# Optimization experiments

Measured on AMD Instinct MI355X. Metric: run time of the kernel, lower is better.

Reference implementation:

```python
import jax, jax.numpy as jnp
import numpy as np

WIDTH = 384  # reconstruction grid is WIDTH x WIDTH


def _conv2d(x, w, b, pad):
    y = jax.lax.conv_general_dilated(
        x, w, window_strides=(1, 1), padding=[(pad, pad), (pad, pad)],
        dimension_numbers=('NCHW', 'OIHW', 'NCHW'))
    return y + b[None, :, None, None]


def _backproject(sino, angles, width):
    """Pixel-driven flat-detector fan-beam backprojection with linear interp.
    torch-radon FanBeam defaults: src_dist = det_dist = det_count,
    det_spacing = (src_dist + det_dist) / src_dist.
    sino: [B, C, A, D] -> image [B, C, width, width]."""
    B, C, A, D = sino.shape
    dsrc = float(D)
    ddet = float(D)
    spacing = (dsrc + ddet) / dsrc  # = 2.0
    c = jnp.arange(width, dtype=sino.dtype) - (width - 1) / 2.0
    X = c[None, None, :]   # [1,1,W] image x
    Y = c[None, :, None]   # [1,W,1] image y
    cb = jnp.cos(angles)[:, None, None]  # [A,1,1]
    sb = jnp.sin(angles)[:, None, None]
    px = cb * X + sb * Y    # pixel coords in rotated (source) frame, [A,W,W]
    py = -sb * X + cb * Y
    # fractional detector coordinate of the ray source->pixel
    s = px * ((dsrc + ddet) / spacing) / (dsrc + py) + (D - 1) / 2.0
    i0 = jnp.floor(s)
    frac = s - i0
    i0 = i0.astype(jnp.int32)
    i1 = i0 + 1
    WW = width * width
    w0 = jnp.where((i0 >= 0) & (i0 < D), 1.0 - frac, 0.0).reshape(A, WW)
    w1 = jnp.where((i1 >= 0) & (i1 < D), frac, 0.0).reshape(A, WW)
    i0c = jnp.clip(i0, 0, D - 1).reshape(A, WW)
    i1c = jnp.clip(i1, 0, D - 1).reshape(A, WW)

    def gather(idx):
        return jnp.take_along_axis(
            sino, jnp.broadcast_to(idx[None, None], (B, C, A, WW)), axis=3)

    out = (gather(i0c) * w0 + gather(i1c) * w1).sum(axis=2)  # sum over angles
    return out.reshape(B, C, width, width)


def setup_inputs() -> dict:
    key = jax.random.key(0)
    ks = jax.random.split(key, 5)
    A, D = 192, 576
    sino = jax.random.normal(ks[0], (1, 1, A, D), dtype=jnp.float32)
    angles = (jnp.arange(A, dtype=jnp.float32) * (2.0 * np.pi / A))
    w1 = jax.random.normal(ks[1], (16, 1, 5, 5), dtype=jnp.float32) * 0.05
    b1 = jnp.zeros((16,), dtype=jnp.float32)
    w2 = jax.random.normal(ks[2], (1, 16, 5, 5), dtype=jnp.float32) * 0.05
    b2 = jnp.zeros((1,), dtype=jnp.float32)
    w3 = jax.random.normal(ks[3], (1, 2, 3, 3), dtype=jnp.float32) * 0.05
    b3 = jnp.zeros((1,), dtype=jnp.float32)
    return {"sino": sino, "angles": angles, "w1": w1, "b1": b1,
            "w2": w2, "b2": b2, "w3": w3, "b3": b3}


def reference(sino, angles, w1, b1, w2, b2, w3, b3):
    img = _backproject(sino, angles, WIDTH)
    h = _conv2d(sino, w1, b1, pad=2)
    sino_pred = _conv2d(h, w2, b2, pad=2)
    img_sino = _backproject(sino_pred, angles, WIDTH)
    img_pred = _conv2d(jnp.concatenate([img, img_sino], axis=1), w3, b3, pad=1)
    return (sino_pred, img_sino, img_pred)
```

## Files before the change

kernel.cpp:

```cpp
#include <hip/hip_runtime.h>

#define A_N 192
#define D_N 576
#define W_N 384
#define NPIX (W_N * W_N)
#define NSIN (A_N * D_N)
#define RSTR 580

__global__ __launch_bounds__(256) void conv9_kernel(
    const float* __restrict__ sino, const float* __restrict__ angles,
    const float* __restrict__ w1, const float* __restrict__ b1,
    const float* __restrict__ w2, const float* __restrict__ b2,
    float* __restrict__ sino_pred, float2* __restrict__ inter,
    float4* __restrict__ tab)
{
    __shared__ float t[16][40];
    __shared__ float sw1[400], sw2[400], sb1[16];
    __shared__ float K[625], wsb1[25];
    __shared__ float Wcs[9][81];
    __shared__ float biasc[9];

    int tid = threadIdx.x;
    int byi = blockIdx.x / 18;
    int bxi = blockIdx.x % 18;
    int y0 = byi * 8, x0 = bxi * 32;

    if (blockIdx.x == 0) {
        if (tid < A_N) {
            float s, c;
            sincosf(angles[tid], &s, &c);
            tab[tid] = make_float4(c, s, fmaf(576.f, c, -287.5f * s),
                                         fmaf(576.f, s,  287.5f * c));
        }
        for (int i = tid; i < A_N * 4; i += 256) {
            int a = i >> 2, j = i & 3;
            inter[a * RSTR + (j < 2 ? j : 576 + j)] = make_float2(0.f, 0.f);
        }
    }

    for (int i = tid; i < 640; i += 256) {
        int r = i / 40, c = i - r * 40;
        int gy = y0 - 4 + r, gx = x0 - 4 + c;
        t[r][c] = (gy >= 0 && gy < A_N && gx >= 0 && gx < D_N)
                ? sino[gy * D_N + gx] : 0.f;
    }
    for (int i = tid; i < 400; i += 256) { sw1[i] = w1[i]; sw2[i] = w2[i]; }
    if (tid < 16) sb1[tid] = b1[tid];
    __syncthreads();

    for (int i = tid; i < 625; i += 256) {
        int q = i / 25, r = i - q * 25;
        float acc = 0.f;
        #pragma unroll
        for (int c = 0; c < 16; ++c)
            acc = fmaf(sw2[c * 25 + q], sw1[c * 25 + r], acc);
        K[i] = acc;
    }
    if (tid < 25) {
        float acc = 0.f;
        #pragma unroll
        for (int c = 0; c < 16; ++c) acc = fmaf(sw2[c * 25 + tid], sb1[c], acc);
        wsb1[tid] = acc;
    }
    __syncthreads();

    int ylo = (y0 == 0) ? 0 : 2, yhi = (y0 == A_N - 8) ? 4 : 2;
    int xlo = (x0 == 0) ? 0 : 2, xhi = (x0 == D_N - 32) ? 4 : 2;
    int nx = xhi - xlo + 1;
    int nc = (yhi - ylo + 1) * nx;

    for (int e = tid; e < nc * 81; e += 256) {
        int ci = e / 81, s = e - ci * 81;
        int yc = ylo + ci / nx, xc = xlo + ci % nx;
        int sy = s / 9 - 4, sx = s % 9 - 4;
        float acc = 0.f;
        for (int qy = -2; qy <= 2; ++qy) {
            if ((yc == 0 && qy < 0) || (yc == 1 && qy < -1) ||
                (yc == 3 && qy > 1) || (yc == 4 && qy > 0)) continue;
            int vy = sy - qy; if (vy < -2 || vy > 2) continue;
            for (int qx = -2; qx <= 2; ++qx) {
                if ((xc == 0 && qx < 0) || (xc == 1 && qx < -1) ||
                    (xc == 3 && qx > 1) || (xc == 4 && qx > 0)) continue;
                int vx = sx - qx; if (vx < -2 || vx > 2) continue;
                acc += K[((qy + 2) * 5 + qx + 2) * 25 + (vy + 2) * 5 + (vx + 2)];
            }
        }
        Wcs[ci][s] = acc;
    }
    if (tid < nc) {
        int yc = ylo + tid / nx, xc = xlo + tid % nx;
        float acc = b2[0];
        for (int qy = -2; qy <= 2; ++qy) {
            if ((yc == 0 && qy < 0) || (yc == 1 && qy < -1) ||
                (yc == 3 && qy > 1) || (yc == 4 && qy > 0)) continue;
            for (int qx = -2; qx <= 2; ++qx) {
                if ((xc == 0 && qx < 0) || (xc == 1 && qx < -1) ||
                    (xc == 3 && qx > 1) || (xc == 4 && qx > 0)) continue;
                acc += wsb1[(qy + 2) * 5 + qx + 2];
            }
        }
        biasc[tid] = acc;
    }
    __syncthreads();

    int lr = tid >> 5, lc = tid & 31;
    int gy = y0 + lr, gx = x0 + lc;
    int yc = (gy <= 1) ? gy : ((gy >= A_N - 2) ? (gy - (A_N - 5)) : 2);
    int xc = (gx <= 1) ? gx : ((gx >= D_N - 2) ? (gx - (D_N - 5)) : 2);
    int ci = (yc - ylo) * nx + (xc - xlo);
    float acc = biasc[ci];
    const float* Wp = Wcs[ci];
    #pragma unroll
    for (int sy = 0; sy < 9; ++sy)
        #pragma unroll
        for (int sx = 0; sx < 9; ++sx)
            acc = fmaf(t[lr + sy][lc + sx], Wp[sy * 9 + sx], acc);
    sino_pred[gy * D_N + gx] = acc;
    inter[gy * RSTR + 2 + gx] = make_float2(t[lr + 4][lc + 4], acc);
}

__global__ __launch_bounds__(256) void backproject2_kernel(
    const float2* __restrict__ inter, const float4* __restrict__ tab,
    float* __restrict__ part)
{
    int tid = threadIdx.x;
    int seg = blockIdx.z;
    int a0 = seg * 48;
    int tx = tid & 15, ty = tid >> 4;
    int gx = blockIdx.x * 16 + tx;
    int gy = blockIdx.y * 16 + ty;
    int idx = gy * W_N + gx;
    float X = (float)gx - 191.5f;
    float Y = (float)gy - 191.5f;
    float acc0 = 0.f, acc1 = 0.f;
    const float2* base = inter + (size_t)a0 * RSTR + 2;
    #pragma unroll 4
    for (int i = 0; i < 48; ++i) {
        float4 tb = tab[a0 + i];
        float den = fmaf(tb.x, Y, fmaf(-tb.y, X, 576.f));
        float num = fmaf(tb.z, X, fmaf(tb.w, Y, 165600.f));
        float s   = num * __builtin_amdgcn_rcpf(den);
        float fl  = floorf(s);
        float fr  = s - fl;
        int   i0  = (int)fl;
        bool valid = (unsigned)(i0 + 1) <= 577u;
        float w0 = valid ? (1.f - fr) : 0.f;
        float w1 = valid ? fr : 0.f;
        int ic = min(max(i0, -1), 576);
        float4 v = *reinterpret_cast<const float4*>(base + (size_t)i * RSTR + ic);
        acc0 = fmaf(v.x, w0, fmaf(v.z, w1, acc0));
        acc1 = fmaf(v.y, w0, fmaf(v.w, w1, acc1));
    }
    part[seg * NPIX + idx]       = acc0;
    part[(4 + seg) * NPIX + idx] = acc1;
}

__global__ __launch_bounds__(256) void conv3_kernel(
    const float* __restrict__ part,
    const float* __restrict__ w3, const float* __restrict__ b3,
    float* __restrict__ img_sino, float* __restrict__ img_pred)
{
    __shared__ float t0[10][34], t1[10][34];
    __shared__ float sw[18];
    int tid = threadIdx.x;
    int byi = blockIdx.x / 12, bxi = blockIdx.x % 12;
    int y0 = byi * 8, x0 = bxi * 32;
    for (int i = tid; i < 340; i += 256) {
        int r = i / 34, c = i - r * 34;
        int gy = y0 - 1 + r, gx = x0 - 1 + c;
        float s0 = 0.f, s1 = 0.f;
        if (gy >= 0 && gy < W_N && gx >= 0 && gx < W_N) {
            int g = gy * W_N + gx;
            #pragma unroll
            for (int p = 0; p < 4; ++p) s0 += part[p * NPIX + g];
            #pragma unroll
            for (int p = 4; p < 8; ++p) s1 += part[p * NPIX + g];
        }
        t0[r][c] = s0; t1[r][c] = s1;
    }
    if (tid < 18) sw[tid] = w3[tid];
    __syncthreads();
    int lr = tid >> 5, lc = tid & 31;
    int gy = y0 + lr, gx = x0 + lc;
    int g = gy * W_N + gx;
    img_sino[g] = t1[lr + 1][lc + 1];
    float acc = b3[0];
    #pragma unroll
    for (int dy = 0; dy < 3; ++dy)
        #pragma unroll
        for (int dx = 0; dx < 3; ++dx) {
            acc = fmaf(t0[lr + dy][lc + dx], sw[dy * 3 + dx], acc);
            acc = fmaf(t1[lr + dy][lc + dx], sw[9 + dy * 3 + dx], acc);
        }
    img_pred[g] = acc;
}

extern "C" void kernel_launch(void* const* d_in, const int* in_sizes, int n_in,
                              void* d_out, int out_size, void* d_ws, size_t ws_size,
                              hipStream_t stream) {
    const float* sino   = (const float*)d_in[0];
    const float* angles = (const float*)d_in[1];
    const float* w1     = (const float*)d_in[2];
    const float* b1     = (const float*)d_in[3];
    const float* w2     = (const float*)d_in[4];
    const float* b2     = (const float*)d_in[5];
    const float* w3     = (const float*)d_in[6];
    const float* b3     = (const float*)d_in[7];

    float* out       = (float*)d_out;
    float* sino_pred = out;
    float* img_sino  = out + NSIN;
    float* img_pred  = img_sino + NPIX;

    float2* inter = (float2*)d_ws;
    float4* tab   = (float4*)((char*)d_ws + (size_t)A_N * RSTR * sizeof(float2));
    float*  part  = (float*)((char*)tab + A_N * sizeof(float4));

    conv9_kernel<<<dim3(432), dim3(256), 0, stream>>>(
        sino, angles, w1, b1, w2, b2, sino_pred, inter, tab);
    backproject2_kernel<<<dim3(24, 24, 4), dim3(256), 0, stream>>>(
        inter, tab, part);
    conv3_kernel<<<dim3(576), dim3(256), 0, stream>>>(
        part, w3, b3, img_sino, img_pred);
}
```

Before: 38.49 us.

## Split weight-folding into prep kernel and retile backprojection into 8x8 blocks

Moves the per-block 9x9 composite-kernel folding out of conv9 into a single-block prep kernel that writes all 25 boundary-class kernels to global memory; conv9 blocks now just copy the classes they need. Backprojection switches to 64-thread 8x8 pixel tiles with 2 angle segments of 96, which halves the partial buffers that conv3 must sum. The validity branch is dropped by clamping the index to -2 and relying on zero padding columns. This adds a kernel launch and a serialized single-block prep stage, and the clamp assumes out-of-range taps always land on zeroed padding.

Result: slower. 44.47 us (+15.5%).

```diff
diff --git a/kernel.cpp b/kernel.cpp
--- a/kernel.cpp
+++ b/kernel.cpp
@@ -7,47 +7,19 @@
 #define NSIN (A_N * D_N)
 #define RSTR 580
 
-__global__ __launch_bounds__(256) void conv9_kernel(
-    const float* __restrict__ sino, const float* __restrict__ angles,
+__global__ __launch_bounds__(256) void prep_kernel(
+    const float* __restrict__ angles,
     const float* __restrict__ w1, const float* __restrict__ b1,
     const float* __restrict__ w2, const float* __restrict__ b2,
-    float* __restrict__ sino_pred, float2* __restrict__ inter,
-    float4* __restrict__ tab)
-{
-    __shared__ float t[16][40];
+    float4* __restrict__ tab, float2* __restrict__ inter,
+    float* __restrict__ Wc_g, float* __restrict__ biasc_g)
+{
     __shared__ float sw1[400], sw2[400], sb1[16];
     __shared__ float K[625], wsb1[25];
-    __shared__ float Wcs[9][81];
-    __shared__ float biasc[9];
-
-    int tid = threadIdx.x;
-    int byi = blockIdx.x / 18;
-    int bxi = blockIdx.x % 18;
-    int y0 = byi * 8, x0 = bxi * 32;
-
-    if (blockIdx.x == 0) {
-        if (tid < A_N) {
-            float s, c;
-            sincosf(angles[tid], &s, &c);
-            tab[tid] = make_float4(c, s, fmaf(576.f, c, -287.5f * s),
-                                         fmaf(576.f, s,  287.5f * c));
-        }
-        for (int i = tid; i < A_N * 4; i += 256) {
-            int a = i >> 2, j = i & 3;
-            inter[a * RSTR + (j < 2 ? j : 576 + j)] = make_float2(0.f, 0.f);
-        }
-    }
-
-    for (int i = tid; i < 640; i += 256) {
-        int r = i / 40, c = i - r * 40;
-        int gy = y0 - 4 + r, gx = x0 - 4 + c;
-        t[r][c] = (gy >= 0 && gy < A_N && gx >= 0 && gx < D_N)
-                ? sino[gy * D_N + gx] : 0.f;
-    }
+    int tid = threadIdx.x;
     for (int i = tid; i < 400; i += 256) { sw1[i] = w1[i]; sw2[i] = w2[i]; }
     if (tid < 16) sb1[tid] = b1[tid];
     __syncthreads();
-
     for (int i = tid; i < 625; i += 256) {
         int q = i / 25, r = i - q * 25;
         float acc = 0.f;
@@ -63,15 +35,9 @@
         wsb1[tid] = acc;
     }
     __syncthreads();
-
-    int ylo = (y0 == 0) ? 0 : 2, yhi = (y0 == A_N - 8) ? 4 : 2;
-    int xlo = (x0 == 0) ? 0 : 2, xhi = (x0 == D_N - 32) ? 4 : 2;
-    int nx = xhi - xlo + 1;
-    int nc = (yhi - ylo + 1) * nx;
-
-    for (int e = tid; e < nc * 81; e += 256) {
-        int ci = e / 81, s = e - ci * 81;
-        int yc = ylo + ci / nx, xc = xlo + ci % nx;
+    for (int e = tid; e < 2025; e += 256) {
+        int cl = e / 81, s = e - cl * 81;
+        int yc = cl / 5, xc = cl - yc * 5;
         int sy = s / 9 - 4, sx = s % 9 - 4;
         float acc = 0.f;
         for (int qy = -2; qy <= 2; ++qy) {
@@ -85,10 +51,10 @@
                 acc += K[((qy + 2) * 5 + qx + 2) * 25 + (vy + 2) * 5 + (vx + 2)];
             }
         }
-        Wcs[ci][s] = acc;
-    }
-    if (tid < nc) {
-        int yc = ylo + tid / nx, xc = xlo + tid % nx;
+        Wc_g[e] = acc;
+    }
+    if (tid < 25) {
+        int yc = tid / 5, xc = tid % 5;
         float acc = b2[0];
         for (int qy = -2; qy <= 2; ++qy) {
             if ((yc == 0 && qy < 0) || (yc == 1 && qy < -1) ||
@@ -99,7 +65,51 @@
                 acc += wsb1[(qy + 2) * 5 + qx + 2];
             }
         }
-        biasc[tid] = acc;
+        biasc_g[tid] = acc;
+    }
+    if (tid < A_N) {
+        float s, c;
+        sincosf(angles[tid], &s, &c);
+        tab[tid] = make_float4(c, s, fmaf(576.f, c, -287.5f * s),
+                                     fmaf(576.f, s,  287.5f * c));
+    }
+    for (int i = tid; i < A_N * 4; i += 256) {
+        int a = i >> 2, j = i & 3;
+        inter[a * RSTR + (j < 2 ? j : 576 + j)] = make_float2(0.f, 0.f);
+    }
+}
+
+__global__ __launch_bounds__(256) void conv9_kernel(
+    const float* __restrict__ sino,
+    const float* __restrict__ Wc_g, const float* __restrict__ biasc_g,
+    float* __restrict__ sino_pred, float2* __restrict__ inter)
+{
+    __shared__ float t[16][40];
+    __shared__ float Wcs[9][81];
+    __shared__ float biasc[9];
+    int tid = threadIdx.x;
+    int byi = blockIdx.x / 18;
+    int bxi = blockIdx.x % 18;
+    int y0 = byi * 8, x0 = bxi * 32;
+
+    for (int i = tid; i < 640; i += 256) {
+        int r = i / 40, c = i - r * 40;
+        int gy = y0 - 4 + r, gx = x0 - 4 + c;
+        t[r][c] = (gy >= 0 && gy < A_N && gx >= 0 && gx < D_N)
+                ? sino[gy * D_N + gx] : 0.f;
+    }
+    int ylo = (y0 == 0) ? 0 : 2, yhi = (y0 == A_N - 8) ? 4 : 2;
+    int xlo = (x0 == 0) ? 0 : 2, xhi = (x0 == D_N - 32) ? 4 : 2;
+    int nx = xhi - xlo + 1;
+    int nc = (yhi - ylo + 1) * nx;
+    for (int e = tid; e < nc * 81; e += 256) {
+        int ci = e / 81, s = e - ci * 81;
+        int yc = ylo + ci / nx, xc = xlo + ci % nx;
+        Wcs[ci][s] = Wc_g[(yc * 5 + xc) * 81 + s];
+    }
+    if (tid < nc) {
+        int yc = ylo + tid / nx, xc = xlo + tid % nx;
+        biasc[tid] = biasc_g[yc * 5 + xc];
     }
     __syncthreads();
 
@@ -119,40 +129,36 @@
     inter[gy * RSTR + 2 + gx] = make_float2(t[lr + 4][lc + 4], acc);
 }
 
-__global__ __launch_bounds__(256) void backproject2_kernel(
+__global__ __launch_bounds__(64) void backproject2_kernel(
     const float2* __restrict__ inter, const float4* __restrict__ tab,
     float* __restrict__ part)
 {
     int tid = threadIdx.x;
     int seg = blockIdx.z;
-    int a0 = seg * 48;
-    int tx = tid & 15, ty = tid >> 4;
-    int gx = blockIdx.x * 16 + tx;
-    int gy = blockIdx.y * 16 + ty;
+    int a0 = seg * 96;
+    int tx = tid & 7, ty = tid >> 3;
+    int gx = blockIdx.x * 8 + tx;
+    int gy = blockIdx.y * 8 + ty;
     int idx = gy * W_N + gx;
     float X = (float)gx - 191.5f;
     float Y = (float)gy - 191.5f;
     float acc0 = 0.f, acc1 = 0.f;
     const float2* base = inter + (size_t)a0 * RSTR + 2;
     #pragma unroll 4
-    for (int i = 0; i < 48; ++i) {
+    for (int i = 0; i < 96; ++i) {
         float4 tb = tab[a0 + i];
         float den = fmaf(tb.x, Y, fmaf(-tb.y, X, 576.f));
         float num = fmaf(tb.z, X, fmaf(tb.w, Y, 165600.f));
         float s   = num * __builtin_amdgcn_rcpf(den);
         float fl  = floorf(s);
         float fr  = s - fl;
-        int   i0  = (int)fl;
-        bool valid = (unsigned)(i0 + 1) <= 577u;
-        float w0 = valid ? (1.f - fr) : 0.f;
-        float w1 = valid ? fr : 0.f;
-        int ic = min(max(i0, -1), 576);
+        int   ic  = min(max((int)fl, -2), 576);
         float4 v = *reinterpret_cast<const float4*>(base + (size_t)i * RSTR + ic);
-        acc0 = fmaf(v.x, w0, fmaf(v.z, w1, acc0));
-        acc1 = fmaf(v.y, w0, fmaf(v.w, w1, acc1));
+        acc0 = fmaf(v.x, 1.f - fr, fmaf(v.z, fr, acc0));
+        acc1 = fmaf(v.y, 1.f - fr, fmaf(v.w, fr, acc1));
     }
     part[seg * NPIX + idx]       = acc0;
-    part[(4 + seg) * NPIX + idx] = acc1;
+    part[(2 + seg) * NPIX + idx] = acc1;
 }
 
 __global__ __launch_bounds__(256) void conv3_kernel(
@@ -165,18 +171,17 @@
     int tid = threadIdx.x;
     int byi = blockIdx.x / 12, bxi = blockIdx.x % 12;
     int y0 = byi * 8, x0 = bxi * 32;
+    const float* p0a = part;
+    const float* p0b = part + NPIX;
+    const float* p1a = part + 2 * NPIX;
+    const float* p1b = part + 3 * NPIX;
     for (int i = tid; i < 340; i += 256) {
         int r = i / 34, c = i - r * 34;
         int gy = y0 - 1 + r, gx = x0 - 1 + c;
-        float s0 = 0.f, s1 = 0.f;
-        if (gy >= 0 && gy < W_N && gx >= 0 && gx < W_N) {
-            int g = gy * W_N + gx;
-            #pragma unroll
-            for (int p = 0; p < 4; ++p) s0 += part[p * NPIX + g];
-            #pragma unroll
-            for (int p = 4; p < 8; ++p) s1 += part[p * NPIX + g];
-        }
-        t0[r][c] = s0; t1[r][c] = s1;
+        bool in = (gy >= 0 && gy < W_N && gx >= 0 && gx < W_N);
+        int g = gy * W_N + gx;
+        t0[r][c] = in ? p0a[g] + p0b[g] : 0.f;
+        t1[r][c] = in ? p1a[g] + p1b[g] : 0.f;
     }
     if (tid < 18) sw[tid] = w3[tid];
     __syncthreads();
@@ -212,13 +217,18 @@
     float* img_sino  = out + NSIN;
     float* img_pred  = img_sino + NPIX;
 
-    float2* inter = (float2*)d_ws;
-    float4* tab   = (float4*)((char*)d_ws + (size_t)A_N * RSTR * sizeof(float2));
-    float*  part  = (float*)((char*)tab + A_N * sizeof(float4));
-
+    char* ws = (char*)d_ws;
+    float2* inter  = (float2*)ws;
+    float4* tab    = (float4*)(ws + (size_t)A_N * RSTR * 8);
+    float*  Wc_g   = (float*)((char*)tab + A_N * 16);
+    float*  biasc_g= Wc_g + 2025;
+    float*  part   = biasc_g + 25 + 2;
+
+    prep_kernel<<<dim3(1), dim3(256), 0, stream>>>(
+        angles, w1, b1, w2, b2, tab, inter, Wc_g, biasc_g);
     conv9_kernel<<<dim3(432), dim3(256), 0, stream>>>(
-        sino, angles, w1, b1, w2, b2, sino_pred, inter, tab);
-    backproject2_kernel<<<dim3(24, 24, 4), dim3(256), 0, stream>>>(
+        sino, Wc_g, biasc_g, sino_pred, inter);
+    backproject2_kernel<<<dim3(48, 48, 2), dim3(64), 0, stream>>>(
         inter, tab, part);
     conv3_kernel<<<dim3(576), dim3(256), 0, stream>>>(
         part, w3, b3, img_sino, img_pred);
```
